# Kernel tuning notes

Hardware: AMD Instinct MI355X
Metric: run time of the kernel (lower is better)

Reference implementation:

```python
import jax, jax.numpy as jnp
import numpy as np

H, W, A, C = 200, 704, 2, 256   # BEV grid, anchors, feature channels
NC, K = 4, 20000                # peer CAVs, selected anchors per CAV
REG = 7 * A                     # reg head channels


def setup_inputs() -> dict:
    key = jax.random.key(0)
    ks = jax.random.split(key, 8)
    feat = jax.random.normal(ks[0], (1, C, H, W), jnp.float32)
    cls_w = jax.random.normal(ks[1], (A, C), jnp.float32) * 0.02
    cls_b = jnp.zeros((A,), jnp.float32)
    reg_w = jax.random.normal(ks[2], (REG, C), jnp.float32) * 0.02
    reg_b = jnp.zeros((REG,), jnp.float32)
    psm_v2x = jax.random.normal(ks[3], (NC, K), jnp.float32)
    rm_v2x = jax.random.normal(ks[4], (NC, 7 * K), jnp.float32)
    scores_v2x = jax.random.uniform(ks[5], (NC, K), jnp.float32, 0.3, 1.0)
    flat = A * H * W
    idx = []
    for i in range(NC):  # unique sorted flat indices per CAV (masked_select semantics)
        perm = jax.random.permutation(jax.random.fold_in(ks[6], i), flat)[:K]
        idx.append(jnp.sort(perm))
    mask_idx = jnp.stack(idx).astype(jnp.int32)
    # mask_reg = mask.repeat(1,7,1,1): indices tile with offsets r*A*H*W
    offs = (jnp.arange(7) * flat).astype(jnp.int32)
    mask_reg_idx = (mask_idx[:, None, :] + offs[None, :, None]).reshape(NC, 7 * K)
    return {
        'spatial_features_2d': feat, 'cls_w': cls_w, 'cls_b': cls_b,
        'reg_w': reg_w, 'reg_b': reg_b, 'psm_v2x': psm_v2x, 'rm_v2x': rm_v2x,
        'scores_v2x': scores_v2x, 'mask_idx': mask_idx, 'mask_reg_idx': mask_reg_idx,
    }


def _restore(vals, idx, shape):
    # restore_tensor: scatter compacted values into zeros at flat indices, per CAV
    n = vals.shape[0]
    flat = int(np.prod(shape))
    out = jnp.zeros((n, flat), vals.dtype)
    out = out.at[jnp.arange(n)[:, None], idx].set(vals)
    return out.reshape((n,) + shape)


def reference(spatial_features_2d, cls_w, cls_b, reg_w, reg_b,
              psm_v2x, rm_v2x, scores_v2x, mask_idx, mask_reg_idx):
    # 1x1 conv heads
    psm_single = jnp.einsum('bchw,ac->bahw', spatial_features_2d, cls_w) + cls_b[None, :, None, None]
    rm_single = jnp.einsum('bchw,rc->brhw', spatial_features_2d, reg_w) + reg_b[None, :, None, None]
    prob = jax.nn.sigmoid(psm_single)
    # scatter-restore peer CAV results onto the BEV grid
    r_psm = _restore(psm_v2x, mask_idx, (A, H, W))        # [NC,A,H,W]
    r_scores = _restore(scores_v2x, mask_idx, (A, H, W))
    r_rm = _restore(rm_v2x, mask_reg_idx, (REG, H, W))    # [NC,14,H,W]
    psm_all = jnp.concatenate([psm_single, r_psm], axis=0)      # [1+NC,A,H,W]
    prob_all = jnp.concatenate([prob, r_scores], axis=0)
    rm_all = jnp.concatenate([rm_single, r_rm], axis=0)         # [1+NC,14,H,W]
    # per-cell winning CAV by score, then gather psm/rm from the winner
    cav = jnp.argmax(prob_all, axis=0)                    # [A,H,W]
    psm = jnp.take_along_axis(psm_all, cav[None], axis=0) # [1,A,H,W]
    cav_reg = jnp.tile(cav, (7, 1, 1))                    # [14,H,W]
    rm = jnp.take_along_axis(rm_all, cav_reg[None], axis=0)  # [1,14,H,W]
    return psm, rm
```

## Files before the change

kernel.cpp:

```cpp
#include <hip/hip_runtime.h>

#define HH 200
#define WW 704
#define HW (HH * WW)
#define HW4 (HW / 4)
#define AHW (2 * HW)
#define CC 256
#define NCAV 4
#define KK 20000
#define NJ 16

typedef unsigned int u32;

__global__ void scatter_best(const int* __restrict__ mask_idx,
                             const float* __restrict__ scores,
                             u32* __restrict__ winmap) {
    int t = blockIdx.x * blockDim.x + threadIdx.x;
    if (t >= NCAV * KK) return;
    int x = mask_idx[t];
    int n = t / KK;
    union { float f; u32 u; } s;
    s.f = scores[t];
    u32 pack = ((s.u - 0x3E800000u) << 7) | (u32)(3 - n);
    atomicMax(winmap + x, pack);
}

__device__ __forceinline__ int bsearch_row(const int* __restrict__ row, int x) {
    int lo = 0, hi = KK;
    while (lo < hi) {
        int mid = (lo + hi) >> 1;
        if (row[mid] < x) lo = mid + 1; else hi = mid;
    }
    return lo;
}

__global__ __launch_bounds__(64) void head_select(
    const float4* __restrict__ feat4,
    const float* __restrict__ cls_w,
    const float* __restrict__ reg_w,
    const float* __restrict__ cls_b,
    const float* __restrict__ reg_b,
    const float* __restrict__ psm_v2x,
    const float* __restrict__ rm_v2x,
    const int* __restrict__ mask_idx,
    const u32* __restrict__ winmap,
    float* __restrict__ out) {
    __shared__ float w_lds[CC * NJ];

    int tid = threadIdx.x;
    for (int i = tid; i < CC * NJ; i += 64) {
        int j = i >> 8, c = i & 255;
        w_lds[c * NJ + j] = (j < 2) ? cls_w[j * CC + c] : reg_w[(j - 2) * CC + c];
    }
    __syncthreads();

    int q = blockIdx.x * 64 + tid;
    int pos = q * 4;

    float acc[4][NJ];
#pragma unroll
    for (int j = 0; j < NJ; ++j) {
        float b = (j < 2) ? cls_b[j] : reg_b[j - 2];
        acc[0][j] = b; acc[1][j] = b; acc[2][j] = b; acc[3][j] = b;
    }

#pragma unroll 8
    for (int c = 0; c < CC; ++c) {
        float4 f = feat4[c * HW4 + q];
        const float4* wv = (const float4*)&w_lds[c * NJ];
        float w[NJ];
        *(float4*)&w[0]  = wv[0];
        *(float4*)&w[4]  = wv[1];
        *(float4*)&w[8]  = wv[2];
        *(float4*)&w[12] = wv[3];
#pragma unroll
        for (int j = 0; j < NJ; ++j) {
            acc[0][j] += f.x * w[j];
            acc[1][j] += f.y * w[j];
            acc[2][j] += f.z * w[j];
            acc[3][j] += f.w * w[j];
        }
    }

    float4* out4 = (float4*)out;
#pragma unroll
    for (int a = 0; a < 2; ++a) {
        float ps[4], rm[7][4];
#pragma unroll
        for (int e = 0; e < 4; ++e) {
            float p = acc[e][a];
            float prob = 1.0f / (1.0f + expf(-p));
            int x = a * HW + pos + e;
            u32 win = winmap[x];
            float sc = 0.0f;
            if (win != 0u) {
                union { u32 u; float f; } v;
                v.u = (win >> 7) + 0x3E800000u;
                sc = v.f;
            }
            if (sc > prob) {
                int n = 3 - (int)(win & 3u);
                int k = bsearch_row(mask_idx + n * KK, x);
                ps[e] = psm_v2x[n * KK + k];
#pragma unroll
                for (int r = 0; r < 7; ++r)
                    rm[r][e] = rm_v2x[n * (7 * KK) + r * KK + k];
            } else {
                ps[e] = p;
#pragma unroll
                for (int r = 0; r < 7; ++r)
                    rm[r][e] = acc[e][2 + 2 * r + a];
            }
        }
        out4[a * HW4 + q] = make_float4(ps[0], ps[1], ps[2], ps[3]);
#pragma unroll
        for (int r = 0; r < 7; ++r)
            out4[(AHW / 4) + (2 * r + a) * HW4 + q] =
                make_float4(rm[r][0], rm[r][1], rm[r][2], rm[r][3]);
    }
}

extern "C" void kernel_launch(void* const* d_in, const int* in_sizes, int n_in,
                              void* d_out, int out_size, void* d_ws, size_t ws_size,
                              hipStream_t stream) {
    const float* feat    = (const float*)d_in[0];
    const float* cls_w   = (const float*)d_in[1];
    const float* cls_b   = (const float*)d_in[2];
    const float* reg_w   = (const float*)d_in[3];
    const float* reg_b   = (const float*)d_in[4];
    const float* psm_v2x = (const float*)d_in[5];
    const float* rm_v2x  = (const float*)d_in[6];
    const float* scores  = (const float*)d_in[7];
    const int* mask_idx  = (const int*)d_in[8];

    const size_t win_bytes = (size_t)AHW * sizeof(u32);
    u32* winmap = (ws_size >= win_bytes) ? (u32*)d_ws : (u32*)d_in[9];

    hipMemsetAsync(winmap, 0, win_bytes, stream);

    scatter_best<<<(NCAV * KK + 255) / 256, 256, 0, stream>>>(mask_idx, scores, winmap);
    head_select<<<HW4 / 64, 64, 0, stream>>>(
        (const float4*)feat, cls_w, reg_w, cls_b, reg_b,
        psm_v2x, rm_v2x, mask_idx, winmap, (float*)d_out);
}
```

Baseline: 298.4 us.

## Halve per-thread pixels and double-buffer feature loads in head kernel

Each thread now handles two pixels (float2) instead of four, which doubles the grid size and shrinks the accumulator registers. The channel loop is restructured into a register double-buffered software pipeline: the next eight channels' feature values are loaded while the current eight are being multiplied. The launch bound now also specifies one block per SM. The aim is more memory-level parallelism and latency hiding on the HBM-bound feature read, at the cost of narrower 8-byte loads and stores, redundant LDS weight reads per pixel, and possibly lower occupancy from the extra buffer registers.

After: 249.4 us. -16.4%, faster.

```diff
diff --git a/kernel.cpp b/kernel.cpp
--- a/kernel.cpp
+++ b/kernel.cpp
@@ -3,12 +3,13 @@
 #define HH 200
 #define WW 704
 #define HW (HH * WW)
-#define HW4 (HW / 4)
+#define HW2 (HW / 2)
 #define AHW (2 * HW)
 #define CC 256
 #define NCAV 4
 #define KK 20000
 #define NJ 16
+#define UPIPE 8
 
 typedef unsigned int u32;
 
@@ -34,8 +35,8 @@
     return lo;
 }
 
-__global__ __launch_bounds__(64) void head_select(
-    const float4* __restrict__ feat4,
+__global__ __launch_bounds__(64, 1) void head_select(
+    const float2* __restrict__ feat2,
     const float* __restrict__ cls_w,
     const float* __restrict__ reg_w,
     const float* __restrict__ cls_b,
@@ -55,39 +56,67 @@
     __syncthreads();
 
     int q = blockIdx.x * 64 + tid;
-    int pos = q * 4;
+    int pos = q * 2;
 
-    float acc[4][NJ];
+    float acc[2][NJ];
 #pragma unroll
     for (int j = 0; j < NJ; ++j) {
         float b = (j < 2) ? cls_b[j] : reg_b[j - 2];
-        acc[0][j] = b; acc[1][j] = b; acc[2][j] = b; acc[3][j] = b;
+        acc[0][j] = b; acc[1][j] = b;
     }
 
-#pragma unroll 8
-    for (int c = 0; c < CC; ++c) {
-        float4 f = feat4[c * HW4 + q];
-        const float4* wv = (const float4*)&w_lds[c * NJ];
-        float w[NJ];
-        *(float4*)&w[0]  = wv[0];
-        *(float4*)&w[4]  = wv[1];
-        *(float4*)&w[8]  = wv[2];
-        *(float4*)&w[12] = wv[3];
+    const float2* fp = feat2 + q;
+
+    float2 A[UPIPE], B[UPIPE];
 #pragma unroll
-        for (int j = 0; j < NJ; ++j) {
-            acc[0][j] += f.x * w[j];
-            acc[1][j] += f.y * w[j];
-            acc[2][j] += f.z * w[j];
-            acc[3][j] += f.w * w[j];
+    for (int u = 0; u < UPIPE; ++u) A[u] = fp[u * HW2];
+
+    for (int cb = 0; cb < CC; cb += 2 * UPIPE) {
+#pragma unroll
+        for (int u = 0; u < UPIPE; ++u) B[u] = fp[(cb + UPIPE + u) * HW2];
+#pragma unroll
+        for (int u = 0; u < UPIPE; ++u) {
+            int c = cb + u;
+            const float4* wv = (const float4*)&w_lds[c * NJ];
+            float w[NJ];
+            *(float4*)&w[0]  = wv[0];
+            *(float4*)&w[4]  = wv[1];
+            *(float4*)&w[8]  = wv[2];
+            *(float4*)&w[12] = wv[3];
+#pragma unroll
+            for (int j = 0; j < NJ; ++j) {
+                acc[0][j] += A[u].x * w[j];
+                acc[1][j] += A[u].y * w[j];
+            }
+        }
+#pragma unroll
+        for (int u = 0; u < UPIPE; ++u) {
+            int cn = cb + 2 * UPIPE + u;
+            A[u] = fp[(cn < CC ? cn : 0) * HW2];
+        }
+#pragma unroll
+        for (int u = 0; u < UPIPE; ++u) {
+            int c = cb + UPIPE + u;
+            const float4* wv = (const float4*)&w_lds[c * NJ];
+            float w[NJ];
+            *(float4*)&w[0]  = wv[0];
+            *(float4*)&w[4]  = wv[1];
+            *(float4*)&w[8]  = wv[2];
+            *(float4*)&w[12] = wv[3];
+#pragma unroll
+            for (int j = 0; j < NJ; ++j) {
+                acc[0][j] += B[u].x * w[j];
+                acc[1][j] += B[u].y * w[j];
+            }
         }
     }
 
-    float4* out4 = (float4*)out;
+    float2* out2 = (float2*)out;
 #pragma unroll
     for (int a = 0; a < 2; ++a) {
-        float ps[4], rm[7][4];
+        float ps[2], rm[7][2];
 #pragma unroll
-        for (int e = 0; e < 4; ++e) {
+        for (int e = 0; e < 2; ++e) {
             float p = acc[e][a];
             float prob = 1.0f / (1.0f + expf(-p));
             int x = a * HW + pos + e;
@@ -112,11 +141,10 @@
                     rm[r][e] = acc[e][2 + 2 * r + a];
             }
         }
-        out4[a * HW4 + q] = make_float4(ps[0], ps[1], ps[2], ps[3]);
+        out2[a * HW2 + q] = make_float2(ps[0], ps[1]);
 #pragma unroll
         for (int r = 0; r < 7; ++r)
-            out4[(AHW / 4) + (2 * r + a) * HW4 + q] =
-                make_float4(rm[r][0], rm[r][1], rm[r][2], rm[r][3]);
+            out2[HW + (2 * r + a) * HW2 + q] = make_float2(rm[r][0], rm[r][1]);
     }
 }
 
@@ -139,7 +167,7 @@
     hipMemsetAsync(winmap, 0, win_bytes, stream);
 
     scatter_best<<<(NCAV * KK + 255) / 256, 256, 0, stream>>>(mask_idx, scores, winmap);
-    head_select<<<HW4 / 64, 64, 0, stream>>>(
-        (const float4*)feat, cls_w, reg_w, cls_b, reg_b,
+    head_select<<<HW2 / 64, 64, 0, stream>>>(
+        (const float2*)feat, cls_w, reg_w, cls_b, reg_b,
         psm_v2x, rm_v2x, mask_idx, winmap, (float*)d_out);
 }
```
